# Optimization experiments

Hardware: AMD Instinct MI355X
Metric: run time of the kernel (lower is better)

## Reference

```python
import jax, jax.numpy as jnp
import numpy as np
import math

# Model config (see init_kwargs)
E = 1024   # emb_size
H = 8      # ffwd_num_head
D = 128    # ffwd_head_size (E == H*D)
NE = 16    # ffwd_num_expert
A = 2      # ffwd_num_expert_active
S = 256    # ffwd_expert_size
B = 2      # batch_size_fwd
T = 2048   # context_window
NUM_BLOCK = 12


def setup_inputs() -> dict:
    key = jax.random.key(0)
    ks = jax.random.split(key, 5)
    x = jax.random.normal(ks[0], (B, T, E), jnp.float32)
    # fc_in_fused: Linear(E, 4E+NE, bias=False), torch weight shape (out,in)
    w_in = 0.02 * jax.random.normal(ks[1], (4 * E + NE, E), jnp.float32)
    # fc_out_fused: Linear(2E, E), std 0.02/sqrt(num_block)
    w_out = (0.02 / math.sqrt(NUM_BLOCK)) * jax.random.normal(ks[2], (E, 2 * E), jnp.float32)
    # k_ffwd/v_ffwd: original (1,H,NE*S,D); stored here as (NE,H,S,D) for per-expert scan
    k_ffwd = 0.02 * jax.random.normal(ks[3], (NE, H, S, D), jnp.float32)
    v_ffwd = 0.02 * jax.random.normal(ks[4], (NE, H, S, D), jnp.float32)
    return {"x": x, "w_in": w_in, "w_out": w_out, "k_ffwd": k_ffwd, "v_ffwd": v_ffwd}


def _rope(t):
    # Standard half-split RoPE, base 10000. t: (B,T,H,D)
    half = t.shape[-1] // 2
    inv_freq = 1.0 / (10000.0 ** (jnp.arange(half, dtype=jnp.float32) / half))
    ang = jnp.arange(t.shape[1], dtype=jnp.float32)[:, None] * inv_freq  # (T, half)
    cos = jnp.cos(ang)[None, :, None, :]
    sin = jnp.sin(ang)[None, :, None, :]
    t1, t2 = t[..., :half], t[..., half:]
    return jnp.concatenate([t1 * cos - t2 * sin, t1 * sin + t2 * cos], axis=-1)


def reference(x, w_in, w_out, k_ffwd, v_ffwd):
    Bx, Tx, _ = x.shape
    h = x @ w_in.T  # (B,T,4E+NE)
    q_f, q_a, k_a, v_a, router_logits = jnp.split(h, [E, 2 * E, 3 * E, 4 * E], axis=-1)

    # top-k routing (order of the k slots is irrelevant: outputs are summed)
    gate_logits, assign = jax.lax.top_k(router_logits, A)  # (B,T,A)
    gate = jax.nn.sigmoid(gate_logits)

    # --- attention half: causal softmax attention, scale 1/sqrt(D), with RoPE ---
    q = _rope(q_a.reshape(Bx, Tx, H, D))
    k = _rope(k_a.reshape(Bx, Tx, H, D))
    v = v_a.reshape(Bx, Tx, H, D)
    scores = jnp.einsum('bqhd,bkhd->bhqk', q, k) / math.sqrt(D)
    causal = jnp.tril(jnp.ones((Tx, Tx), dtype=bool))
    scores = jnp.where(causal, scores, -jnp.inf)
    p = jax.nn.softmax(scores, axis=-1)
    attn_out = jnp.einsum('bhqk,bkhd->bqhd', p, v).reshape(Bx, Tx, E)

    # --- MoE-FFN half, expressed as attention with score_mod log1p(gelu):
    # exp(lse)*softmax recovers sum_s (1+gelu(q.k_s)) v_s; subtracting sum_s v_s
    # leaves sum_s gelu(q.k_s) v_s over the assigned expert's slots. ---
    qf = q_f.reshape(Bx, Tx, H, D)

    def step(acc, ekv):
        e, ke, ve = ekv  # ke, ve: (H,S,D)
        s = jnp.einsum('bthd,hsd->bths', qf, ke)
        a = jax.nn.gelu(s, approximate=False)  # torch F.gelu default = exact erf
        o = jnp.einsum('bths,hsd->bthd', a, ve)
        g = jnp.sum(jnp.where(assign == e, gate, 0.0), axis=-1)  # (B,T)
        return acc + g[..., None, None] * o, None

    acc0 = jnp.zeros((Bx, Tx, H, D), x.dtype)
    ffwd_out, _ = jax.lax.scan(step, acc0, (jnp.arange(NE), k_ffwd, v_ffwd))
    ffwd_out = ffwd_out.reshape(Bx, Tx, E)

    out = jnp.concatenate([attn_out, ffwd_out], axis=-1) @ w_out.T  # (B,T,E)
    return out
```

## Files before the change

### kernel.cpp

```cpp
#include <hip/hip_runtime.h>
#include <hip/hip_bf16.h>
#include <math.h>

#define E 1024
#define NEXP 16
#define HH 8
#define DD 128
#define SS 256
#define BB 2
#define TT 2048
#define BT 4096

typedef __attribute__((ext_vector_type(8))) short bf16x8;
typedef __attribute__((ext_vector_type(4))) float f32x4;

#define GLDS16(g, s) __builtin_amdgcn_global_load_lds( \
    (const __attribute__((address_space(1))) void*)(g), \
    (__attribute__((address_space(3))) void*)(s), 16, 0, 0)

__device__ __forceinline__ ushort f2b(float f) {
    union { float f; unsigned u; } v; v.f = f;
    unsigned r = (v.u + 0x7FFFu + ((v.u >> 16) & 1u)) >> 16;
    return (ushort)r;
}
__device__ __forceinline__ float b2f(ushort u) {
    union { unsigned u; float f; } v; v.u = ((unsigned)u) << 16;
    return v.f;
}
__device__ __forceinline__ float gelu_fast(float x) {
    float u2 = x * x;
    float tu = x * (1.5957691216f + 0.0713548163f * u2);
    float e = __expf(tu);
    float sig = 1.f - __builtin_amdgcn_rcpf(e + 1.f);
    return x * sig;
}

__global__ __launch_bounds__(256) void prep(
    const float* __restrict__ w_in, const float* __restrict__ w_out,
    const float* __restrict__ kf, const float* __restrict__ vf,
    const float* __restrict__ x,
    ushort* __restrict__ wib, ushort* __restrict__ wob,
    ushort* __restrict__ kfb, ushort* __restrict__ vtf,
    float* __restrict__ gval, int* __restrict__ eidx, ushort* __restrict__ xb)
{
    __shared__ float T[64][132];
    const int bx = blockIdx.x;
    const int t = threadIdx.x;

    if (bx >= 3584) {
        const int m = (bx - 3584) * 4 + (t >> 6);
        const int lane = t & 63;

        const float* xp = x + (size_t)m * 1024 + lane * 4;
        float4 xv0 = *(const float4*)(xp);
        float4 xv1 = *(const float4*)(xp + 256);
        float4 xv2 = *(const float4*)(xp + 512);
        float4 xv3 = *(const float4*)(xp + 768);

        {
            const int swrow = (m & 7) << 4;
            char* xrow = (char*)xb + (size_t)m * 2048;
            ushort4 u;
            u.x = f2b(xv0.x); u.y = f2b(xv0.y); u.z = f2b(xv0.z); u.w = f2b(xv0.w);
            *(ushort4*)(xrow + ((lane * 8 + 0 * 512) ^ swrow)) = u;
            u.x = f2b(xv1.x); u.y = f2b(xv1.y); u.z = f2b(xv1.z); u.w = f2b(xv1.w);
            *(ushort4*)(xrow + ((lane * 8 + 1 * 512) ^ swrow)) = u;
            u.x = f2b(xv2.x); u.y = f2b(xv2.y); u.z = f2b(xv2.z); u.w = f2b(xv2.w);
            *(ushort4*)(xrow + ((lane * 8 + 2 * 512) ^ swrow)) = u;
            u.x = f2b(xv3.x); u.y = f2b(xv3.y); u.z = f2b(xv3.z); u.w = f2b(xv3.w);
            *(ushort4*)(xrow + ((lane * 8 + 3 * 512) ^ swrow)) = u;
        }

        float p[16];
        #pragma unroll
        for (int e = 0; e < 16; ++e) {
            const float* wp = w_in + (size_t)(4096 + e) * 1024 + lane * 4;
            float4 w0 = *(const float4*)(wp);
            float4 w1 = *(const float4*)(wp + 256);
            float4 w2 = *(const float4*)(wp + 512);
            float4 w3 = *(const float4*)(wp + 768);
            float s0 = xv0.x * w0.x + xv0.y * w0.y + xv0.z * w0.z + xv0.w * w0.w;
            float s1 = xv1.x * w1.x + xv1.y * w1.y + xv1.z * w1.z + xv1.w * w1.w;
            float s2 = xv2.x * w2.x + xv2.y * w2.y + xv2.z * w2.z + xv2.w * w2.w;
            float s3 = xv3.x * w3.x + xv3.y * w3.y + xv3.z * w3.z + xv3.w * w3.w;
            p[e] = (s0 + s1) + (s2 + s3);
        }
        #pragma unroll
        for (int d = 1; d < 64; d <<= 1) {
            #pragma unroll
            for (int e = 0; e < 16; ++e)
                p[e] += __shfl_xor(p[e], d);
        }
        float best = -1e30f; int bi = 0;
        #pragma unroll
        for (int e = 0; e < 16; ++e)
            if (p[e] > best) { best = p[e]; bi = e; }
        float best2 = -1e30f; int bi2 = 0;
        #pragma unroll
        for (int e = 0; e < 16; ++e)
            if (e != bi && p[e] > best2) { best2 = p[e]; bi2 = e; }

        if (lane == 0) {
            gval[m * 2 + 0] = 1.f / (1.f + __expf(-best));
            gval[m * 2 + 1] = 1.f / (1.f + __expf(-best2));
            eidx[m * 2 + 0] = bi;
            eidx[m * 2 + 1] = bi2;
        }
        return;
    }

    if (bx < 3072) {
        const float* in;
        ushort* outp;
        int kshift, i;
        if (bx < 2048) { in = w_in;  outp = wib; kshift = 10; i = (bx * 256 + t) * 8; }
        else           { in = w_out; outp = wob; kshift = 11; i = ((bx - 2048) * 256 + t) * 8; }
        int row = i >> kshift;
        int colb = (i - (row << kshift)) * 2;
        float4 f0 = *(const float4*)(in + i);
        float4 f1 = *(const float4*)(in + i + 4);
        ushort4 u0, u1;
        u0.x = f2b(f0.x); u0.y = f2b(f0.y); u0.z = f2b(f0.z); u0.w = f2b(f0.w);
        u1.x = f2b(f1.x); u1.y = f2b(f1.y); u1.z = f2b(f1.z); u1.w = f2b(f1.w);
        char* dst = (char*)outp + ((size_t)row << (kshift + 1)) + (colb ^ ((row & 7) << 4));
        *(ushort4*)dst = u0;
        *(ushort4*)(dst + 8) = u1;
        return;
    }

    const int idx = bx - 3072;
    const int st = idx & 3, eh = idx >> 2;
    const int s0 = st * 64;
    const float* kbp = kf + (size_t)eh * SS * DD + (size_t)s0 * DD;
    const float* vbp = vf + (size_t)eh * SS * DD + (size_t)s0 * DD;
    for (int i = t; i < 64 * 32; i += 256) {
        int r = i >> 5, c4 = i & 31;
        float4 f = *(const float4*)(kbp + (size_t)r * DD + c4 * 4);
        ushort4 u;
        u.x = f2b(f.x); u.y = f2b(f.y); u.z = f2b(f.z); u.w = f2b(f.w);
        *(ushort4*)((char*)kfb + ((size_t)eh * 256 + s0 + r) * 256 + ((c4 * 8) ^ ((r & 7) << 4))) = u;
    }
    for (int i = t; i < 64 * 32; i += 256) {
        int r = i >> 5, c4 = i & 31;
        float4 f = *(const float4*)(vbp + (size_t)r * DD + c4 * 4);
        T[r][c4 * 4 + 0] = f.x; T[r][c4 * 4 + 1] = f.y;
        T[r][c4 * 4 + 2] = f.z; T[r][c4 * 4 + 3] = f.w;
    }
    __syncthreads();
    int g = t >> 4, fr = t & 15;
    #pragma unroll
    for (int dd = 0; dd < 8; ++dd) {
        int d = g + dd * 16;
        ushort4 u;
        u.x = f2b(T[4 * fr + 0][d]); u.y = f2b(T[4 * fr + 1][d]);
        u.z = f2b(T[4 * fr + 2][d]); u.w = f2b(T[4 * fr + 3][d]);
        size_t ob = ((size_t)eh * 128 + d) * 512 + s0 * 2;
        *(ushort4*)((char*)vtf + ob + ((8 * fr) ^ ((d & 7) << 4))) = u;
    }
}

template<int BF16OUT>
__global__ __launch_bounds__(256) void gemm_bf16(
    const ushort* __restrict__ A, int lda,
    const ushort* __restrict__ B, int ldb,
    void* __restrict__ Cv, int ldc, int K)
{
    __shared__ ushort As[128 * 64];
    __shared__ ushort Bs[128 * 64];
    const int t = threadIdx.x;
    const int l = t & 63, w = t >> 6;
    const int m0 = blockIdx.y * 128, n0 = blockIdx.x * 128;
    const int wr = w >> 1, wc = w & 1;
    const int fr = l & 15, fg = l >> 4;

    const int srow = w * 32 + (l >> 3);
    const int sboff = (l & 7) * 16;
    const char* Ag = (const char*)A + ((size_t)(m0 + srow) * lda) * 2 + sboff;
    const char* Bg = (const char*)B + ((size_t)(n0 + srow) * ldb) * 2 + sboff;
    const int aswz = (fr & 7) << 4;

    f32x4 acc[4][4];
    #pragma unroll
    for (int i = 0; i < 4; ++i)
        #pragma unroll
        for (int j = 0; j < 4; ++j) { acc[i][j][0]=0.f; acc[i][j][1]=0.f; acc[i][j][2]=0.f; acc[i][j][3]=0.f; }

    for (int k0b = 0; k0b < K * 2; k0b += 128) {
        #pragma unroll
        for (int i = 0; i < 4; ++i) {
            GLDS16(Ag + (size_t)(i * 8) * lda * 2 + k0b, (char*)As + (w * 32 + i * 8) * 128);
            GLDS16(Bg + (size_t)(i * 8) * ldb * 2 + k0b, (char*)Bs + (w * 32 + i * 8) * 128);
        }
        __syncthreads();
        #pragma unroll
        for (int ksub = 0; ksub < 2; ++ksub) {
            bf16x8 a[4], b[4];
            #pragma unroll
            for (int mi = 0; mi < 4; ++mi)
                a[mi] = *(const bf16x8*)((const char*)As + (wr * 64 + mi * 16 + fr) * 128 + ((ksub * 64 + fg * 16) ^ aswz));
            #pragma unroll
            for (int ni = 0; ni < 4; ++ni)
                b[ni] = *(const bf16x8*)((const char*)Bs + (wc * 64 + ni * 16 + fr) * 128 + ((ksub * 64 + fg * 16) ^ aswz));
            #pragma unroll
            for (int mi = 0; mi < 4; ++mi)
                #pragma unroll
                for (int ni = 0; ni < 4; ++ni)
                    acc[mi][ni] = __builtin_amdgcn_mfma_f32_16x16x32_bf16(a[mi], b[ni], acc[mi][ni], 0, 0, 0);
        }
        __syncthreads();
    }
    #pragma unroll
    for (int mi = 0; mi < 4; ++mi)
        #pragma unroll
        for (int ni = 0; ni < 4; ++ni) {
            const int row = m0 + wr * 64 + mi * 16 + fg * 4;
            const int col = n0 + wc * 64 + ni * 16 + fr;
            #pragma unroll
            for (int r = 0; r < 4; ++r) {
                if (BF16OUT)
                    ((ushort*)Cv)[(size_t)(row + r) * ldc + col] = f2b(acc[mi][ni][r]);
                else
                    ((float*)Cv)[(size_t)(row + r) * ldc + col] = acc[mi][ni][r];
            }
        }
}

__global__ __launch_bounds__(256) void gemm1_fused(
    const ushort* __restrict__ A, const ushort* __restrict__ B,
    ushort* __restrict__ hbq,
    ushort* __restrict__ qb, ushort* __restrict__ kb,
    ushort* __restrict__ vtb,
    const int* __restrict__ eidx,
    int* __restrict__ counts, int* __restrict__ plist)
{
    __shared__ ushort sh[128 * 128];
    const int lin = blockIdx.x;
    const int t = threadIdx.x;

    if (lin >= 1024) {
        int* ish = (int*)sh;
        const int e = lin - 1024;
        const int w = t >> 6, lane = t & 63;
        const int base = w * 2048;

        int cnt = 0;
        for (int c = 0; c < 2048; c += 64) {
            bool match = (eidx[base + c + lane] == e);
            unsigned long long mask = __ballot(match);
            cnt += __popcll(mask);
        }
        if (lane == 0) ish[w] = cnt;
        __syncthreads();
        int off = 0;
        #pragma unroll
        for (int i = 0; i < 4; ++i) if (i < w) off += ish[i];
        for (int c = 0; c < 2048; c += 64) {
            bool match = (eidx[base + c + lane] == e);
            unsigned long long mask = __ballot(match);
            int lpre = __popcll(mask & ((1ull << lane) - 1ull));
            if (match) plist[e * BT + off + lpre] = base + c + lane;
            off += __popcll(mask);
        }
        if (t == 0) counts[e] = ish[0] + ish[1] + ish[2] + ish[3];
        return;
    }

    ushort* As = sh;
    ushort* Bs = sh + 128 * 64;
    const int l = t & 63, w = t >> 6;
    const int bxn = lin & 31, by = lin >> 5;
    const int m0 = by * 128, n0 = bxn * 128;
    const int wr = w >> 1, wc = w & 1;
    const int fr = l & 15, fg = l >> 4;

    const int srow = w * 32 + (l >> 3);
    const int sboff = (l & 7) * 16;
    const char* Ag = (const char*)A + ((size_t)(m0 + srow) * 1024) * 2 + sboff;
    const char* Bg = (const char*)B + ((size_t)(n0 + srow) * 1024) * 2 + sboff;
    const int aswz = (fr & 7) << 4;

    f32x4 acc[4][4];
    #pragma unroll
    for (int i = 0; i < 4; ++i)
        #pragma unroll
        for (int j = 0; j < 4; ++j) { acc[i][j][0]=0.f; acc[i][j][1]=0.f; acc[i][j][2]=0.f; acc[i][j][3]=0.f; }

    for (int k0b = 0; k0b < 2048; k0b += 128) {
        #pragma unroll
        for (int i = 0; i < 4; ++i) {
            GLDS16(Ag + (size_t)(i * 8) * 2048 + k0b, (char*)As + (w * 32 + i * 8) * 128);
            GLDS16(Bg + (size_t)(i * 8) * 2048 + k0b, (char*)Bs + (w * 32 + i * 8) * 128);
        }
        __syncthreads();
        #pragma unroll
        for (int ksub = 0; ksub < 2; ++ksub) {
            bf16x8 a[4], b[4];
            #pragma unroll
            for (int mi = 0; mi < 4; ++mi)
                a[mi] = *(const bf16x8*)((const char*)As + (wr * 64 + mi * 16 + fr) * 128 + ((ksub * 64 + fg * 16) ^ aswz));
            #pragma unroll
            for (int ni = 0; ni < 4; ++ni)
                b[ni] = *(const bf16x8*)((const char*)Bs + (wc * 64 + ni * 16 + fr) * 128 + ((ksub * 64 + fg * 16) ^ aswz));
            #pragma unroll
            for (int mi = 0; mi < 4; ++mi)
                #pragma unroll
                for (int ni = 0; ni < 4; ++ni)
                    acc[mi][ni] = __builtin_amdgcn_mfma_f32_16x16x32_bf16(a[mi], b[ni], acc[mi][ni], 0, 0, 0);
        }
        __syncthreads();
    }

    const int region = bxn >> 3;
    const int hd = bxn & 7;

    if (region == 0) {
        #pragma unroll
        for (int mi = 0; mi < 4; ++mi)
            #pragma unroll
            for (int ni = 0; ni < 4; ++ni) {
                const int row = m0 + wr * 64 + mi * 16 + fg * 4;
                const int col = n0 + wc * 64 + ni * 16 + fr;
                #pragma unroll
                for (int r = 0; r < 4; ++r)
                    hbq[(size_t)(row + r) * 1024 + col] = f2b(acc[mi][ni][r]);
            }
    } else if (region == 3) {
        #pragma unroll
        for (int mi = 0; mi < 4; ++mi) {
            const int rowg = m0 + wr * 64 + mi * 16 + fg * 4;
            const int tok = rowg & 2047, bt = rowg >> 11;
            const int bh = bt * 8 + hd;
            #pragma unroll
            for (int ni = 0; ni < 4; ++ni) {
                const int d = wc * 64 + ni * 16 + fr;
                ushort4 u;
                u.x = f2b(acc[mi][ni][0]); u.y = f2b(acc[mi][ni][1]);
                u.z = f2b(acc[mi][ni][2]); u.w = f2b(acc[mi][ni][3]);
                char* dst = (char*)vtb + (size_t)(bh * 128 + d) * 4096
                          + (tok >> 6) * 128 + ((2 * (tok & 63)) ^ ((d & 7) << 4));
                *(ushort4*)dst = u;
            }
        }
    } else {
        #pragma unroll
        for (int mi = 0; mi < 4; ++mi)
            #pragma unroll
            for (int ni = 0; ni < 4; ++ni) {
                const int rl = wr * 64 + mi * 16 + fg * 4;
                const int cl = wc * 64 + ni * 16 + fr;
                #pragma unroll
                for (int r = 0; r < 4; ++r)
                    sh[(rl + r) * 128 + cl] = f2b(acc[mi][ni][r]);
            }
        __syncthreads();
        ushort* outb = (region == 1) ? qb : kb;
        #pragma unroll
        for (int it = 0; it < 4; ++it) {
            const int item = it * 256 + t;
            const int rloc = item >> 3, g = item & 7;
            const int rowg = m0 + rloc;
            const int tok = rowg & 2047, bt = rowg >> 11;
            const int sw = (tok & 7) << 4;
            char* rowbase = (char*)outb + ((size_t)((bt * 8 + hd) * 2048 + tok)) * 256;
            ushort lo[8], hi[8];
            #pragma unroll
            for (int jj = 0; jj < 8; ++jj) {
                const int j = g * 8 + jj;
                float t1 = b2f(sh[rloc * 128 + j]);
                float t2 = b2f(sh[rloc * 128 + 64 + j]);
                float invf = __expf(-(float)j * (9.210340371976184f / 64.f));
                float ang = (float)tok * invf;
                float s, c;
                sincosf(ang, &s, &c);
                lo[jj] = f2b(t1 * c - t2 * s);
                hi[jj] = f2b(t1 * s + t2 * c);
            }
            *(ushort4*)(rowbase + ((16 * g) ^ sw))        = *(ushort4*)&lo[0];
            *(ushort4*)(rowbase + (((16 * g) ^ sw) + 8))  = *(ushort4*)&lo[4];
            *(ushort4*)(rowbase + ((16 * g + 128) ^ sw))       = *(ushort4*)&hi[0];
            *(ushort4*)(rowbase + (((16 * g + 128) ^ sw) + 8)) = *(ushort4*)&hi[4];
        }
    }
}

__global__ __launch_bounds__(512, 1) void attn_mfma(
    const ushort* __restrict__ qb, const ushort* __restrict__ kb,
    const ushort* __restrict__ vtb, ushort* __restrict__ catb)
{
    __shared__ ushort Ks[2][128 * 128];
    __shared__ ushort Vs[2][128 * 128];
    __shared__ ushort Ps[8][16 * 72];
    __shared__ float  LlS[8][16];

    const int t = threadIdx.x, l = t & 63, w = t >> 6;
    const int fr = l & 15, fg = l >> 4;
    const int wl = w & 3, hh = w >> 2;
    const int lin = blockIdx.x;
    const int bh = (lin & 7) * 2 + (lin >> 7);
    const int tpair = (lin >> 3) & 15;
    const int swz = (fr & 7) << 4;
    ushort* Pw = (ushort*)Ps[w];

    #pragma unroll 1
    for (int pass = 0; pass < 2; ++pass) {
        const int qt = pass ? (31 - tpair) : tpair;
        const int qbase = qt * 64;
        const int nkt = (qt + 2) >> 1;
        const int qg = qbase + wl * 16 + fg * 4;

        bf16x8 qreg[4];
        {
            const char* qrow = (const char*)qb + ((size_t)(bh * 2048 + qbase + wl * 16 + fr)) * 256;
            #pragma unroll
            for (int ks = 0; ks < 4; ++ks)
                qreg[ks] = *(const bf16x8*)(qrow + ((ks * 64 + fg * 16) ^ swz));
        }
        {
            const char* ksrc = (const char*)kb + ((size_t)(bh * 2048 + w * 16)) * 256;
            const char* vsrc = (const char*)vtb + ((size_t)(bh * 128 + w * 16)) * 4096;
            #pragma unroll
            for (int i = 0; i < 4; ++i) {
                GLDS16(ksrc + (size_t)(i * 4 + (l >> 4)) * 256 + (l & 15) * 16,
                       (char*)Ks[0] + (w * 16 + i * 4) * 256);
                GLDS16(vsrc + (size_t)(i * 4 + (l >> 4)) * 4096 + (l & 15) * 16,
                       (char*)Vs[0] + (w * 16 + i * 4) * 256);
            }
        }

        f32x4 po[8];
        #pragma unroll
        for (int i = 0; i < 8; ++i) { po[i][0]=0.f; po[i][1]=0.f; po[i][2]=0.f; po[i][3]=0.f; }
        float lrow[4] = {0.f, 0.f, 0.f, 0.f};

        asm volatile("s_waitcnt vmcnt(0)" ::: "memory");
        __syncthreads();

        for (int kt = 0; kt < nkt; ++kt) {
            const int cur = kt & 1;
            if (kt + 1 < nkt) {
                const int kvn = (kt + 1) * 128;
                const char* ksrc = (const char*)kb + ((size_t)(bh * 2048 + kvn + w * 16)) * 256;
                const char* vsrc = (const char*)vtb + ((size_t)(bh * 128 + w * 16)) * 4096 + kvn * 2;
                #pragma unroll
                for (int i = 0; i < 4; ++i) {
                    GLDS16(ksrc + (size_t)(i * 4 + (l >> 4)) * 256 + (l & 15) * 16,
                           (char*)Ks[cur ^ 1] + (w * 16 + i * 4) * 256);
                    GLDS16(vsrc + (size_t)(i * 4 + (l >> 4)) * 4096 + (l & 15) * 16,
                           (char*)Vs[cur ^ 1] + (w * 16 + i * 4) * 256);
                }
            }
            const int kvb = kt * 128;

            f32x4 s[4];
            #pragma unroll
            for (int i = 0; i < 4; ++i) { s[i][0]=0.f; s[i][1]=0.f; s[i][2]=0.f; s[i][3]=0.f; }
            __builtin_amdgcn_s_setprio(1);
            #pragma unroll
            for (int ks = 0; ks < 4; ++ks) {
                #pragma unroll
                for (int fn = 0; fn < 4; ++fn) {
                    const int brow = hh * 64 + fn * 16 + fr;
                    bf16x8 bb = *(const bf16x8*)((const char*)Ks[cur] + brow * 256 + ((ks * 64 + fg * 16) ^ swz));
                    s[fn] = __builtin_amdgcn_mfma_f32_16x16x32_bf16(qreg[ks], bb, s[fn], 0, 0, 0);
                }
            }
            __builtin_amdgcn_s_setprio(0);

            const int colbase = kvb + hh * 64;
            const bool needmask = (colbase + 64 > qbase + wl * 16);
            float ps[4] = {0.f, 0.f, 0.f, 0.f};
            #pragma unroll
            for (int fn = 0; fn < 4; ++fn)
                #pragma unroll
                for (int r = 0; r < 4; ++r) {
                    float v = s[fn][r] * 0.08838834764831845f;
                    bool masked = needmask && (colbase + fn * 16 + fr > qg + r);
                    float p = masked ? 0.f : __expf(v);
                    ps[r] += p;
                    Pw[(fg * 4 + r) * 72 + fn * 16 + fr] = f2b(p);
                }
            #pragma unroll
            for (int r = 0; r < 4; ++r) {
                float s2 = ps[r];
                s2 += __shfl_xor(s2, 1);
                s2 += __shfl_xor(s2, 2);
                s2 += __shfl_xor(s2, 4);
                s2 += __shfl_xor(s2, 8);
                lrow[r] += s2;
            }

            asm volatile("s_waitcnt lgkmcnt(0)" ::: "memory");
            __builtin_amdgcn_sched_barrier(0);

            __builtin_amdgcn_s_setprio(1);
            #pragma unroll
            for (int ks2 = 0; ks2 < 2; ++ks2) {
                bf16x8 pa = *(const bf16x8*)((const char*)Pw + fr * 144 + ks2 * 64 + fg * 16);
                #pragma unroll
                for (int fn2 = 0; fn2 < 8; ++fn2) {
                    const int vrow = fn2 * 16 + fr;
                    bf16x8 bv = *(const bf16x8*)((const char*)Vs[cur] + vrow * 256 + ((hh * 128 + ks2 * 64 + fg * 16) ^ swz));
                    po[fn2] = __builtin_amdgcn_mfma_f32_16x16x32_bf16(pa, bv, po[fn2], 0, 0, 0);
                }
            }
            __builtin_amdgcn_s_setprio(0);

            asm volatile("s_waitcnt vmcnt(0)" ::: "memory");
            __syncthreads();
        }

        if (fr == 0) {
            #pragma unroll
            for (int r = 0; r < 4; ++r)
                LlS[w][fg * 4 + r] = lrow[r];
        }
        __syncthreads();
        float linv[4];
        #pragma unroll
        for (int r = 0; r < 4; ++r)
            linv[r] = 1.f / (lrow[r] + LlS[w ^ 4][fg * 4 + r]);
        float* PO = (float*)&Ks[0][0];
        if (hh == 1) {
            #pragma unroll
            for (int fn2 = 0; fn2 < 8; ++fn2)
                #pragma unroll
                for (int r = 0; r < 4; ++r)
                    PO[(wl * 16 + fg * 4 + r) * 128 + fn2 * 16 + fr] = po[fn2][r];
        }
        __syncthreads();
        if (hh == 0) {
            const int mg = (bh >> 3) * 2048 + qbase + wl * 16 + fg * 4;
            #pragma unroll
            for (int r = 0; r < 4; ++r) {
                const int rswz = ((mg + r) & 7) << 4;
                #pragma unroll
                for (int fn2 = 0; fn2 < 8; ++fn2) {
                    float v = po[fn2][r] + PO[(wl * 16 + fg * 4 + r) * 128 + fn2 * 16 + fr];
                    int colb = ((bh & 7) * 128 + fn2 * 16 + fr) * 2;
                    *(ushort*)((char*)catb + (size_t)(mg + r) * 4096 + (colb ^ rswz)) = f2b(v * linv[r]);
                }
            }
        }
        __syncthreads();
    }
}

__global__ __launch_bounds__(256, 1) void ffn_mfma2(
    const ushort* __restrict__ hbq,
    const float* __restrict__ gv,
    const int* __restrict__ counts,
    const int* __restrict__ plist,
    const ushort* __restrict__ kfb, const ushort* __restrict__ vtf,
    ushort* __restrict__ pairout)
{
    __shared__ ushort Ks[256 * 128];
    __shared__ ushort Vs[128 * 256];
    __shared__ ushort Qs[64 * 128];
    __shared__ ushort Ps[4][16 * 72];

    const int t = threadIdx.x, l = t & 63, w = t >> 6;
    const int fr = l & 15, fg = l >> 4;
    const int half = blockIdx.x, hd = blockIdx.y, e = blockIdx.z;
    const int eh = e * HH + hd;
    const int n_e = counts[e];

    {
        const char* kbase = (const char*)kfb + (size_t)eh * 65536;
        const char* vbase = (const char*)vtf + (size_t)eh * 65536;
        #pragma unroll
        for (int i = 0; i < 16; ++i) {
            GLDS16(kbase + (w * 64 + i * 4) * 256 + l * 16, (char*)Ks + (w * 64 + i * 4) * 256);
            GLDS16(vbase + w * 16384 + i * 1024 + l * 16, (char*)Vs + w * 16384 + i * 1024);
        }
    }
    __syncthreads();

    const int arow = w * 16 + fr;
    const int aswz = (arow & 7) << 4;
    ushort* Pw = (ushort*)Ps[w];
    const int rl4 = l >> 4;
    const int lb = (l & 15) * 16;

    for (int tb = half * 64; tb < n_e; tb += 128) {
        #pragma unroll
        for (int i = 0; i < 4; ++i) {
            int row = w * 16 + i * 4 + rl4;
            int gr = tb + row;
            int p = plist[e * BT + min(gr, n_e - 1)];
            int m = p >> 1;
            const char* src = (const char*)hbq + (size_t)m * 2048 + hd * 256 + (lb ^ ((row & 7) << 4));
            GLDS16(src, (char*)Qs + (w * 16 + i * 4) * 256);
        }
        asm volatile("s_waitcnt vmcnt(0)" ::: "memory");

        f32x4 po[8];
        #pragma unroll
        for (int i = 0; i < 8; ++i) { po[i][0]=0.f; po[i][1]=0.f; po[i][2]=0.f; po[i][3]=0.f; }

        #pragma unroll
        for (int kt = 0; kt < 4; ++kt) {
            const int kvb = kt * 64;
            f32x4 sA[4];
            #pragma unroll
            for (int i = 0; i < 4; ++i) { sA[i][0]=0.f; sA[i][1]=0.f; sA[i][2]=0.f; sA[i][3]=0.f; }
            #pragma unroll
            for (int ks = 0; ks < 4; ++ks) {
                bf16x8 aa = *(const bf16x8*)((const char*)Qs + arow * 256 + ((ks * 64 + fg * 16) ^ aswz));
                #pragma unroll
                for (int fn = 0; fn < 4; ++fn) {
                    const int brow = kvb + fn * 16 + fr;
                    bf16x8 bb = *(const bf16x8*)((const char*)Ks + brow * 256 + ((ks * 64 + fg * 16) ^ ((brow & 7) << 4)));
                    sA[fn] = __builtin_amdgcn_mfma_f32_16x16x32_bf16(aa, bb, sA[fn], 0, 0, 0);
                }
            }
            #pragma unroll
            for (int fn = 0; fn < 4; ++fn)
                #pragma unroll
                for (int r = 0; r < 4; ++r)
                    Pw[(fg * 4 + r) * 72 + fn * 16 + fr] = f2b(gelu_fast(sA[fn][r]));
            asm volatile("s_waitcnt lgkmcnt(0)" ::: "memory");
            #pragma unroll
            for (int ks2 = 0; ks2 < 2; ++ks2) {
                bf16x8 pa = *(const bf16x8*)((const char*)Pw + fr * 144 + ks2 * 64 + fg * 16);
                #pragma unroll
                for (int fn2 = 0; fn2 < 8; ++fn2) {
                    const int vrow = fn2 * 16 + fr;
                    bf16x8 bv = *(const bf16x8*)((const char*)Vs + vrow * 512 + kt * 128 + ((ks2 * 64 + fg * 16) ^ ((vrow & 7) << 4)));
                    po[fn2] = __builtin_amdgcn_mfma_f32_16x16x32_bf16(pa, bv, po[fn2], 0, 0, 0);
                }
            }
        }
        const int rloc = w * 16 + fg * 4;
        #pragma unroll
        for (int r = 0; r < 4; ++r) {
            int gr = tb + rloc + r;
            if (gr < n_e) {
                int p = plist[e * BT + gr];
                float g = gv[p];
                #pragma unroll
                for (int fn2 = 0; fn2 < 8; ++fn2)
                    pairout[(size_t)p * 1024 + hd * DD + fn2 * 16 + fr] = f2b(g * po[fn2][r]);
            }
        }
    }
}

__global__ void combine_kernel(const ushort* __restrict__ po, ushort* __restrict__ catb)
{
    int i = blockIdx.x * blockDim.x + threadIdx.x;
    if (i >= BT * 128) return;
    int m = i >> 7, c = i & 127;
    const ushort* a = po + (size_t)(2 * m) * 1024 + c * 8;
    const ushort* b = po + (size_t)(2 * m + 1) * 1024 + c * 8;
    ushort4 a0 = *(const ushort4*)a, a1 = *(const ushort4*)(a + 4);
    ushort4 b0 = *(const ushort4*)b, b1 = *(const ushort4*)(b + 4);
    ushort4 o0, o1;
    o0.x = f2b(b2f(a0.x) + b2f(b0.x)); o0.y = f2b(b2f(a0.y) + b2f(b0.y));
    o0.z = f2b(b2f(a0.z) + b2f(b0.z)); o0.w = f2b(b2f(a0.w) + b2f(b0.w));
    o1.x = f2b(b2f(a1.x) + b2f(b1.x)); o1.y = f2b(b2f(a1.y) + b2f(b1.y));
    o1.z = f2b(b2f(a1.z) + b2f(b1.z)); o1.w = f2b(b2f(a1.w) + b2f(b1.w));
    char* dst = (char*)catb + (size_t)m * 4096 + 2048 + ((c * 16) ^ ((m & 7) << 4));
    *(ushort4*)dst = o0;
    *(ushort4*)(dst + 8) = o1;
}

extern "C" void kernel_launch(void* const* d_in, const int* in_sizes, int n_in,
                              void* d_out, int out_size, void* d_ws, size_t ws_size,
                              hipStream_t stream)
{
    const float* x     = (const float*)d_in[0];
    const float* w_in  = (const float*)d_in[1];
    const float* w_out = (const float*)d_in[2];
    const float* kf    = (const float*)d_in[3];
    const float* vf    = (const float*)d_in[4];
    float* out = (float*)d_out;

    char* W = (char*)d_ws;
    ushort* hbq     = (ushort*)(W + 0);
    ushort* xb      = (ushort*)(W + 33554432);
    ushort* wib     = (ushort*)(W + 41943040);
    ushort* wob     = (ushort*)(W + 50331648);
    ushort* qb2     = (ushort*)(W + 54525952);
    ushort* kb2     = (ushort*)(W + 62914560);
    ushort* vtb     = (ushort*)(W + 71303168);
    ushort* catb    = (ushort*)(W + 79691776);
    ushort* pairout = (ushort*)(W + 96468992);
    float*  gv      = (float*)(W + 113246208);
    int*    counts  = (int*)(W + 113278976);
    int*    plist   = (int*)(W + 113279040);
    int*    eidx    = (int*)(W + 113541184);
    ushort* kfb     = (ushort*)(W + 113573952);
    ushort* vtf     = (ushort*)(W + 121962560);

    prep<<<4608, 256, 0, stream>>>(w_in, w_out, kf, vf, x,
                                   wib, wob, kfb, vtf, gv, eidx, xb);

    gemm1_fused<<<1040, 256, 0, stream>>>(xb, wib, hbq, qb2, kb2, vtb,
                                          eidx, counts, plist);

    attn_mfma<<<dim3(256), 512, 0, stream>>>(qb2, kb2, vtb, catb);

    ffn_mfma2<<<dim3(2, HH, NEXP), 256, 0, stream>>>(hbq, gv, counts, plist, kfb, vtf, pairout);
    combine_kernel<<<2048, 256, 0, stream>>>(pairout, catb);

    gemm_bf16<0><<<dim3(8, 32), 256, 0, stream>>>(catb, 2048, wob, 2048, out, 1024, 2048);
}
```

Before: 212.3 us.

## Fuse FFN, combine and output GEMM into one cooperative kernel with grid syncs

Merges the MoE-FFN expert kernel, the pair-combine kernel and the final output GEMM into a single cooperative launch of 256 blocks. Grid-wide syncs separate the phases, and the GEMM reuses the FFN's shared memory. This removes two kernel launches and the gaps between them. In exchange it adds two grid barriers and fixes the grid at 256 blocks with one block per CU, which limits the GEMM phase's latency hiding.

```diff
diff --git a/kernel.cpp b/kernel.cpp
--- a/kernel.cpp
+++ b/kernel.cpp
@@ -1,6 +1,9 @@
 #include <hip/hip_runtime.h>
 #include <hip/hip_bf16.h>
+#include <hip/hip_cooperative_groups.h>
 #include <math.h>
+
+namespace cg = cooperative_groups;
 
 #define E 1024
 #define NEXP 16
@@ -159,72 +162,6 @@
     }
 }
 
-template<int BF16OUT>
-__global__ __launch_bounds__(256) void gemm_bf16(
-    const ushort* __restrict__ A, int lda,
-    const ushort* __restrict__ B, int ldb,
-    void* __restrict__ Cv, int ldc, int K)
-{
-    __shared__ ushort As[128 * 64];
-    __shared__ ushort Bs[128 * 64];
-    const int t = threadIdx.x;
-    const int l = t & 63, w = t >> 6;
-    const int m0 = blockIdx.y * 128, n0 = blockIdx.x * 128;
-    const int wr = w >> 1, wc = w & 1;
-    const int fr = l & 15, fg = l >> 4;
-
-    const int srow = w * 32 + (l >> 3);
-    const int sboff = (l & 7) * 16;
-    const char* Ag = (const char*)A + ((size_t)(m0 + srow) * lda) * 2 + sboff;
-    const char* Bg = (const char*)B + ((size_t)(n0 + srow) * ldb) * 2 + sboff;
-    const int aswz = (fr & 7) << 4;
-
-    f32x4 acc[4][4];
-    #pragma unroll
-    for (int i = 0; i < 4; ++i)
-        #pragma unroll
-        for (int j = 0; j < 4; ++j) { acc[i][j][0]=0.f; acc[i][j][1]=0.f; acc[i][j][2]=0.f; acc[i][j][3]=0.f; }
-
-    for (int k0b = 0; k0b < K * 2; k0b += 128) {
-        #pragma unroll
-        for (int i = 0; i < 4; ++i) {
-            GLDS16(Ag + (size_t)(i * 8) * lda * 2 + k0b, (char*)As + (w * 32 + i * 8) * 128);
-            GLDS16(Bg + (size_t)(i * 8) * ldb * 2 + k0b, (char*)Bs + (w * 32 + i * 8) * 128);
-        }
-        __syncthreads();
-        #pragma unroll
-        for (int ksub = 0; ksub < 2; ++ksub) {
-            bf16x8 a[4], b[4];
-            #pragma unroll
-            for (int mi = 0; mi < 4; ++mi)
-                a[mi] = *(const bf16x8*)((const char*)As + (wr * 64 + mi * 16 + fr) * 128 + ((ksub * 64 + fg * 16) ^ aswz));
-            #pragma unroll
-            for (int ni = 0; ni < 4; ++ni)
-                b[ni] = *(const bf16x8*)((const char*)Bs + (wc * 64 + ni * 16 + fr) * 128 + ((ksub * 64 + fg * 16) ^ aswz));
-            #pragma unroll
-            for (int mi = 0; mi < 4; ++mi)
-                #pragma unroll
-                for (int ni = 0; ni < 4; ++ni)
-                    acc[mi][ni] = __builtin_amdgcn_mfma_f32_16x16x32_bf16(a[mi], b[ni], acc[mi][ni], 0, 0, 0);
-        }
-        __syncthreads();
-    }
-    #pragma unroll
-    for (int mi = 0; mi < 4; ++mi)
-        #pragma unroll
-        for (int ni = 0; ni < 4; ++ni) {
-            const int row = m0 + wr * 64 + mi * 16 + fg * 4;
-            const int col = n0 + wc * 64 + ni * 16 + fr;
-            #pragma unroll
-            for (int r = 0; r < 4; ++r) {
-                if (BF16OUT)
-                    ((ushort*)Cv)[(size_t)(row + r) * ldc + col] = f2b(acc[mi][ni][r]);
-                else
-                    ((float*)Cv)[(size_t)(row + r) * ldc + col] = acc[mi][ni][r];
-            }
-        }
-}
-
 __global__ __launch_bounds__(256) void gemm1_fused(
     const ushort* __restrict__ A, const ushort* __restrict__ B,
     ushort* __restrict__ hbq,
@@ -545,13 +482,16 @@
     }
 }
 
-__global__ __launch_bounds__(256, 1) void ffn_mfma2(
+__global__ __launch_bounds__(256, 1) void tail_fused(
     const ushort* __restrict__ hbq,
     const float* __restrict__ gv,
     const int* __restrict__ counts,
     const int* __restrict__ plist,
     const ushort* __restrict__ kfb, const ushort* __restrict__ vtf,
-    ushort* __restrict__ pairout)
+    ushort* __restrict__ pairout,
+    ushort* __restrict__ catb,
+    const ushort* __restrict__ wob,
+    float* __restrict__ C)
 {
     __shared__ ushort Ks[256 * 128];
     __shared__ ushort Vs[128 * 256];
@@ -560,108 +500,175 @@
 
     const int t = threadIdx.x, l = t & 63, w = t >> 6;
     const int fr = l & 15, fg = l >> 4;
-    const int half = blockIdx.x, hd = blockIdx.y, e = blockIdx.z;
-    const int eh = e * HH + hd;
-    const int n_e = counts[e];
+    const int lin = blockIdx.x;
 
     {
-        const char* kbase = (const char*)kfb + (size_t)eh * 65536;
-        const char* vbase = (const char*)vtf + (size_t)eh * 65536;
-        #pragma unroll
-        for (int i = 0; i < 16; ++i) {
-            GLDS16(kbase + (w * 64 + i * 4) * 256 + l * 16, (char*)Ks + (w * 64 + i * 4) * 256);
-            GLDS16(vbase + w * 16384 + i * 1024 + l * 16, (char*)Vs + w * 16384 + i * 1024);
-        }
-    }
+        const int half = lin & 1, hd = (lin >> 1) & 7, e = lin >> 4;
+        const int eh = e * HH + hd;
+        const int n_e = counts[e];
+
+        {
+            const char* kbase = (const char*)kfb + (size_t)eh * 65536;
+            const char* vbase = (const char*)vtf + (size_t)eh * 65536;
+            #pragma unroll
+            for (int i = 0; i < 16; ++i) {
+                GLDS16(kbase + (w * 64 + i * 4) * 256 + l * 16, (char*)Ks + (w * 64 + i * 4) * 256);
+                GLDS16(vbase + w * 16384 + i * 1024 + l * 16, (char*)Vs + w * 16384 + i * 1024);
+            }
+        }
+        __syncthreads();
+
+        const int arow = w * 16 + fr;
+        const int aswz = (arow & 7) << 4;
+        ushort* Pw = (ushort*)Ps[w];
+        const int rl4 = l >> 4;
+        const int lb = (l & 15) * 16;
+
+        for (int tb = half * 64; tb < n_e; tb += 128) {
+            #pragma unroll
+            for (int i = 0; i < 4; ++i) {
+                int row = w * 16 + i * 4 + rl4;
+                int gr = tb + row;
+                int p = plist[e * BT + min(gr, n_e - 1)];
+                int m = p >> 1;
+                const char* src = (const char*)hbq + (size_t)m * 2048 + hd * 256 + (lb ^ ((row & 7) << 4));
+                GLDS16(src, (char*)Qs + (w * 16 + i * 4) * 256);
+            }
+            asm volatile("s_waitcnt vmcnt(0)" ::: "memory");
+
+            f32x4 po[8];
+            #pragma unroll
+            for (int i = 0; i < 8; ++i) { po[i][0]=0.f; po[i][1]=0.f; po[i][2]=0.f; po[i][3]=0.f; }
+
+            #pragma unroll
+            for (int kt = 0; kt < 4; ++kt) {
+                const int kvb = kt * 64;
+                f32x4 sA[4];
+                #pragma unroll
+                for (int i = 0; i < 4; ++i) { sA[i][0]=0.f; sA[i][1]=0.f; sA[i][2]=0.f; sA[i][3]=0.f; }
+                #pragma unroll
+                for (int ks = 0; ks < 4; ++ks) {
+                    bf16x8 aa = *(const bf16x8*)((const char*)Qs + arow * 256 + ((ks * 64 + fg * 16) ^ aswz));
+                    #pragma unroll
+                    for (int fn = 0; fn < 4; ++fn) {
+                        const int brow = kvb + fn * 16 + fr;
+                        bf16x8 bb = *(const bf16x8*)((const char*)Ks + brow * 256 + ((ks * 64 + fg * 16) ^ ((brow & 7) << 4)));
+                        sA[fn] = __builtin_amdgcn_mfma_f32_16x16x32_bf16(aa, bb, sA[fn], 0, 0, 0);
+                    }
+                }
+                #pragma unroll
+                for (int fn = 0; fn < 4; ++fn)
+                    #pragma unroll
+                    for (int r = 0; r < 4; ++r)
+                        Pw[(fg * 4 + r) * 72 + fn * 16 + fr] = f2b(gelu_fast(sA[fn][r]));
+                asm volatile("s_waitcnt lgkmcnt(0)" ::: "memory");
+                #pragma unroll
+                for (int ks2 = 0; ks2 < 2; ++ks2) {
+                    bf16x8 pa = *(const bf16x8*)((const char*)Pw + fr * 144 + ks2 * 64 + fg * 16);
+                    #pragma unroll
+                    for (int fn2 = 0; fn2 < 8; ++fn2) {
+                        const int vrow = fn2 * 16 + fr;
+                        bf16x8 bv = *(const bf16x8*)((const char*)Vs + vrow * 512 + kt * 128 + ((ks2 * 64 + fg * 16) ^ ((vrow & 7) << 4)));
+                        po[fn2] = __builtin_amdgcn_mfma_f32_16x16x32_bf16(pa, bv, po[fn2], 0, 0, 0);
+                    }
+                }
+            }
+            const int rloc = w * 16 + fg * 4;
+            #pragma unroll
+            for (int r = 0; r < 4; ++r) {
+                int gr = tb + rloc + r;
+                if (gr < n_e) {
+                    int p = plist[e * BT + gr];
+                    float g = gv[p];
+                    #pragma unroll
+                    for (int fn2 = 0; fn2 < 8; ++fn2)
+                        pairout[(size_t)p * 1024 + hd * DD + fn2 * 16 + fr] = f2b(g * po[fn2][r]);
+                }
+            }
+        }
+    }
+
     __syncthreads();
-
-    const int arow = w * 16 + fr;
-    const int aswz = (arow & 7) << 4;
-    ushort* Pw = (ushort*)Ps[w];
-    const int rl4 = l >> 4;
-    const int lb = (l & 15) * 16;
-
-    for (int tb = half * 64; tb < n_e; tb += 128) {
-        #pragma unroll
-        for (int i = 0; i < 4; ++i) {
-            int row = w * 16 + i * 4 + rl4;
-            int gr = tb + row;
-            int p = plist[e * BT + min(gr, n_e - 1)];
-            int m = p >> 1;
-            const char* src = (const char*)hbq + (size_t)m * 2048 + hd * 256 + (lb ^ ((row & 7) << 4));
-            GLDS16(src, (char*)Qs + (w * 16 + i * 4) * 256);
-        }
-        asm volatile("s_waitcnt vmcnt(0)" ::: "memory");
-
-        f32x4 po[8];
-        #pragma unroll
-        for (int i = 0; i < 8; ++i) { po[i][0]=0.f; po[i][1]=0.f; po[i][2]=0.f; po[i][3]=0.f; }
-
-        #pragma unroll
-        for (int kt = 0; kt < 4; ++kt) {
-            const int kvb = kt * 64;
-            f32x4 sA[4];
-            #pragma unroll
-            for (int i = 0; i < 4; ++i) { sA[i][0]=0.f; sA[i][1]=0.f; sA[i][2]=0.f; sA[i][3]=0.f; }
-            #pragma unroll
-            for (int ks = 0; ks < 4; ++ks) {
-                bf16x8 aa = *(const bf16x8*)((const char*)Qs + arow * 256 + ((ks * 64 + fg * 16) ^ aswz));
-                #pragma unroll
-                for (int fn = 0; fn < 4; ++fn) {
-                    const int brow = kvb + fn * 16 + fr;
-                    bf16x8 bb = *(const bf16x8*)((const char*)Ks + brow * 256 + ((ks * 64 + fg * 16) ^ ((brow & 7) << 4)));
-                    sA[fn] = __builtin_amdgcn_mfma_f32_16x16x32_bf16(aa, bb, sA[fn], 0, 0, 0);
-                }
-            }
-            #pragma unroll
-            for (int fn = 0; fn < 4; ++fn)
+    __threadfence();
+    cg::this_grid().sync();
+
+    {
+        const int g = lin * 256 + t;
+        #pragma unroll
+        for (int it = 0; it < 8; ++it) {
+            int i = g + it * 65536;
+            int m = i >> 7, c = i & 127;
+            const ushort* a = pairout + (size_t)(2 * m) * 1024 + c * 8;
+            const ushort* b = pairout + (size_t)(2 * m + 1) * 1024 + c * 8;
+            ushort4 a0 = *(const ushort4*)a, a1 = *(const ushort4*)(a + 4);
+            ushort4 b0 = *(const ushort4*)b, b1 = *(const ushort4*)(b + 4);
+            ushort4 o0, o1;
+            o0.x = f2b(b2f(a0.x) + b2f(b0.x)); o0.y = f2b(b2f(a0.y) + b2f(b0.y));
+            o0.z = f2b(b2f(a0.z) + b2f(b0.z)); o0.w = f2b(b2f(a0.w) + b2f(b0.w));
+            o1.x = f2b(b2f(a1.x) + b2f(b1.x)); o1.y = f2b(b2f(a1.y) + b2f(b1.y));
+            o1.z = f2b(b2f(a1.z) + b2f(b1.z)); o1.w = f2b(b2f(a1.w) + b2f(b1.w));
+            char* dst = (char*)catb + (size_t)m * 4096 + 2048 + ((c * 16) ^ ((m & 7) << 4));
+            *(ushort4*)dst = o0;
+            *(ushort4*)(dst + 8) = o1;
+        }
+    }
+
+    __threadfence();
+    cg::this_grid().sync();
+
+    {
+        ushort* As = Ks;
+        ushort* Bs = Ks + 128 * 64;
+        const int m0 = (lin >> 3) * 128, n0 = (lin & 7) * 128;
+        const int wr = w >> 1, wc = w & 1;
+
+        const int srow = w * 32 + (l >> 3);
+        const int sboff = (l & 7) * 16;
+        const char* Ag = (const char*)catb + ((size_t)(m0 + srow) * 2048) * 2 + sboff;
+        const char* Bg = (const char*)wob + ((size_t)(n0 + srow) * 2048) * 2 + sboff;
+        const int aswz = (fr & 7) << 4;
+
+        f32x4 acc[4][4];
+        #pragma unroll
+        for (int i = 0; i < 4; ++i)
+            #pragma unroll
+            for (int j = 0; j < 4; ++j) { acc[i][j][0]=0.f; acc[i][j][1]=0.f; acc[i][j][2]=0.f; acc[i][j][3]=0.f; }
+
+        for (int k0b = 0; k0b < 4096; k0b += 128) {
+            #pragma unroll
+            for (int i = 0; i < 4; ++i) {
+                GLDS16(Ag + (size_t)(i * 8) * 4096 + k0b, (char*)As + (w * 32 + i * 8) * 128);
+                GLDS16(Bg + (size_t)(i * 8) * 4096 + k0b, (char*)Bs + (w * 32 + i * 8) * 128);
+            }
+            __syncthreads();
+            #pragma unroll
+            for (int ksub = 0; ksub < 2; ++ksub) {
+                bf16x8 a[4], b[4];
+                #pragma unroll
+                for (int mi = 0; mi < 4; ++mi)
+                    a[mi] = *(const bf16x8*)((const char*)As + (wr * 64 + mi * 16 + fr) * 128 + ((ksub * 64 + fg * 16) ^ aswz));
+                #pragma unroll
+                for (int ni = 0; ni < 4; ++ni)
+                    b[ni] = *(const bf16x8*)((const char*)Bs + (wc * 64 + ni * 16 + fr) * 128 + ((ksub * 64 + fg * 16) ^ aswz));
+                #pragma unroll
+                for (int mi = 0; mi < 4; ++mi)
+                    #pragma unroll
+                    for (int ni = 0; ni < 4; ++ni)
+                        acc[mi][ni] = __builtin_amdgcn_mfma_f32_16x16x32_bf16(a[mi], b[ni], acc[mi][ni], 0, 0, 0);
+            }
+            __syncthreads();
+        }
+        #pragma unroll
+        for (int mi = 0; mi < 4; ++mi)
+            #pragma unroll
+            for (int ni = 0; ni < 4; ++ni) {
+                const int row = m0 + wr * 64 + mi * 16 + fg * 4;
+                const int col = n0 + wc * 64 + ni * 16 + fr;
                 #pragma unroll
                 for (int r = 0; r < 4; ++r)
-                    Pw[(fg * 4 + r) * 72 + fn * 16 + fr] = f2b(gelu_fast(sA[fn][r]));
-            asm volatile("s_waitcnt lgkmcnt(0)" ::: "memory");
-            #pragma unroll
-            for (int ks2 = 0; ks2 < 2; ++ks2) {
-                bf16x8 pa = *(const bf16x8*)((const char*)Pw + fr * 144 + ks2 * 64 + fg * 16);
-                #pragma unroll
-                for (int fn2 = 0; fn2 < 8; ++fn2) {
-                    const int vrow = fn2 * 16 + fr;
-                    bf16x8 bv = *(const bf16x8*)((const char*)Vs + vrow * 512 + kt * 128 + ((ks2 * 64 + fg * 16) ^ ((vrow & 7) << 4)));
-                    po[fn2] = __builtin_amdgcn_mfma_f32_16x16x32_bf16(pa, bv, po[fn2], 0, 0, 0);
-                }
-            }
-        }
-        const int rloc = w * 16 + fg * 4;
-        #pragma unroll
-        for (int r = 0; r < 4; ++r) {
-            int gr = tb + rloc + r;
-            if (gr < n_e) {
-                int p = plist[e * BT + gr];
-                float g = gv[p];
-                #pragma unroll
-                for (int fn2 = 0; fn2 < 8; ++fn2)
-                    pairout[(size_t)p * 1024 + hd * DD + fn2 * 16 + fr] = f2b(g * po[fn2][r]);
-            }
-        }
-    }
-}
-
-__global__ void combine_kernel(const ushort* __restrict__ po, ushort* __restrict__ catb)
-{
-    int i = blockIdx.x * blockDim.x + threadIdx.x;
-    if (i >= BT * 128) return;
-    int m = i >> 7, c = i & 127;
-    const ushort* a = po + (size_t)(2 * m) * 1024 + c * 8;
-    const ushort* b = po + (size_t)(2 * m + 1) * 1024 + c * 8;
-    ushort4 a0 = *(const ushort4*)a, a1 = *(const ushort4*)(a + 4);
-    ushort4 b0 = *(const ushort4*)b, b1 = *(const ushort4*)(b + 4);
-    ushort4 o0, o1;
-    o0.x = f2b(b2f(a0.x) + b2f(b0.x)); o0.y = f2b(b2f(a0.y) + b2f(b0.y));
-    o0.z = f2b(b2f(a0.z) + b2f(b0.z)); o0.w = f2b(b2f(a0.w) + b2f(b0.w));
-    o1.x = f2b(b2f(a1.x) + b2f(b1.x)); o1.y = f2b(b2f(a1.y) + b2f(b1.y));
-    o1.z = f2b(b2f(a1.z) + b2f(b1.z)); o1.w = f2b(b2f(a1.w) + b2f(b1.w));
-    char* dst = (char*)catb + (size_t)m * 4096 + 2048 + ((c * 16) ^ ((m & 7) << 4));
-    *(ushort4*)dst = o0;
-    *(ushort4*)(dst + 8) = o1;
+                    C[(size_t)(row + r) * 1024 + col] = acc[mi][ni][r];
+            }
+    }
 }
 
 extern "C" void kernel_launch(void* const* d_in, const int* in_sizes, int n_in,
@@ -700,8 +707,10 @@
 
     attn_mfma<<<dim3(256), 512, 0, stream>>>(qb2, kb2, vtb, catb);
 
-    ffn_mfma2<<<dim3(2, HH, NEXP), 256, 0, stream>>>(hbq, gv, counts, plist, kfb, vtf, pairout);
-    combine_kernel<<<2048, 256, 0, stream>>>(pairout, catb);
-
-    gemm_bf16<0><<<dim3(8, 32), 256, 0, stream>>>(catb, 2048, wob, 2048, out, 1024, 2048);
+    {
+        void* args[] = {(void*)&hbq, (void*)&gv, (void*)&counts, (void*)&plist,
+                        (void*)&kfb, (void*)&vtf, (void*)&pairout, (void*)&catb,
+                        (void*)&wob, (void*)&out};
+        hipLaunchCooperativeKernel(tail_fused, dim3(256), dim3(256), args, 0u, stream);
+    }
 }
```

After: 333.0 us. 1.57x slower.
